# Kernel tuning notes

Measured on AMD Instinct MI355X. Metric: run time of the kernel, lower is better.

The kernel has to match this reference:

```python
import jax, jax.numpy as jnp
import numpy as np

DIM = 128
HEADS = 4
DIM_HEAD = 32
HIDDEN = HEADS * DIM_HEAD  # 128
B, N = 8, 16384


def setup_inputs() -> dict:
    key = jax.random.key(0)
    k1, k2, k3, k4 = jax.random.split(key, 4)
    x = jax.random.normal(k1, (B, DIM, N), dtype=jnp.float32)
    # Conv1d kernels with kernel_size=1 are just [out, in] matrices
    w_qkv = jax.random.normal(k2, (3 * HIDDEN, DIM), dtype=jnp.float32) * (1.0 / np.sqrt(DIM))
    w_out = jax.random.normal(k3, (DIM, HIDDEN), dtype=jnp.float32) * (1.0 / np.sqrt(HIDDEN))
    b_out = jax.random.normal(k4, (DIM,), dtype=jnp.float32) * 0.01
    g = jnp.ones((1, DIM, 1), dtype=jnp.float32)  # RMSNorm gain
    return {"x": x, "w_qkv": w_qkv, "w_out": w_out, "b_out": b_out, "g": g}


def reference(x, w_qkv, w_out, b_out, g):
    b, c, n = x.shape
    scale = DIM_HEAD ** -0.5
    # 1x1 conv projection: [b, 3*hidden, n]
    qkv = jnp.einsum('bcn,oc->bon', x, w_qkv)
    q, k, v = jnp.split(qkv, 3, axis=1)
    # [b, h, d, n]
    q = q.reshape(b, HEADS, DIM_HEAD, n)
    k = k.reshape(b, HEADS, DIM_HEAD, n)
    v = v.reshape(b, HEADS, DIM_HEAD, n)
    q = jax.nn.softmax(q, axis=2) * scale   # softmax over feature dim d
    k = jax.nn.softmax(k, axis=3)            # softmax over sequence dim n
    # linear attention: context [b,h,d,e], then expand back over n
    context = jnp.einsum('bhdn,bhen->bhde', k, v)
    out = jnp.einsum('bhde,bhdn->bhen', context, q)
    out = out.reshape(b, HEADS * DIM_HEAD, n)
    # output 1x1 conv with bias
    out = jnp.einsum('bcn,oc->bon', out, w_out) + b_out[None, :, None]
    # RMSNorm over channel dim (F.normalize dim=1, eps=1e-12)
    nrm = jnp.sqrt(jnp.sum(out * out, axis=1, keepdims=True))
    out = out / jnp.maximum(nrm, 1e-12) * g * jnp.sqrt(jnp.asarray(DIM, out.dtype))
    return out
```

## Files before the change

### kernel.cpp

```cpp
#include <hip/hip_runtime.h>
#include <math.h>

typedef unsigned short ushort_t;
typedef unsigned int uint_t;
typedef __attribute__((ext_vector_type(8))) short short8;
typedef __attribute__((ext_vector_type(4))) float f32x4;
typedef __attribute__((ext_vector_type(4))) uint_t uint4v;
typedef __attribute__((ext_vector_type(2))) uint_t uint2v;

#define NSEQ 16384
#define SCALE_Q 0.17677669529663687f
#define RMS_K 11.313708498984761f

__device__ __forceinline__ ushort_t f2bf(float f) {
  uint_t u = __builtin_bit_cast(uint_t, f);
  u += 0x7FFFu + ((u >> 16) & 1u);
  return (ushort_t)(u >> 16);
}
__device__ __forceinline__ uint_t f2bf2(float lo, float hi) {
  return (uint_t)f2bf(lo) | ((uint_t)f2bf(hi) << 16);
}
__device__ __forceinline__ float bf2f(ushort_t u) {
  return __builtin_bit_cast(float, ((uint_t)u) << 16);
}
__device__ __forceinline__ int swz(int row, int col) {
  int slot = (col >> 3) ^ (row & 7);
  int w2 = ((col >> 1) & 3) ^ (((row >> 4) & 1) << 1);
  return row * 128 + slot * 8 + w2 * 2 + (col & 1);
}
__device__ __forceinline__ short8 ldfrag(const ushort_t* lds, int row, int col8, int pp) {
  int slot = (col8 >> 3) ^ (row & 7);
  const uint4v q = *(const uint4v*)&lds[row * 128 + slot * 8];
  uint4v r;
  if (pp) { r.x = q.z; r.y = q.w; r.z = q.x; r.w = q.y; } else { r = q; }
  return __builtin_bit_cast(short8, r);
}
#define MFMA(a, b, c) __builtin_amdgcn_mfma_f32_16x16x32_bf16((a), (b), (c), 0, 0, 0)

__global__ void kP(const float* __restrict__ w_qkv, const float* __restrict__ w_out,
                   ushort_t* __restrict__ wkv_pk, ushort_t* __restrict__ wq_pk,
                   ushort_t* __restrict__ wout_pk) {
  const int i = blockIdx.x * 256 + threadIdx.x;
  const int j = i & 7, lane = (i >> 3) & 63;
  const int l15 = lane & 15, l4 = lane >> 4;
  if (i < 32768) {
    const int rest = i >> 9, Nt = rest & 15, kk = rest >> 4;
    wkv_pk[i] = f2bf(w_qkv[(128 + Nt * 16 + l15) * 128 + kk * 32 + l4 * 8 + j]);
  } else if (i < 49152) {
    const int i2 = i - 32768, rest = i2 >> 9, Nt = rest & 7, kk = rest >> 3;
    wq_pk[i2] = f2bf(w_qkv[(Nt * 16 + l15) * 128 + kk * 32 + l4 * 8 + j]);
  } else if (i < 65536) {
    const int i2 = i - 49152, rest = i2 >> 9, Nt = rest & 7, kk = rest >> 3;
    wout_pk[i2] = f2bf(w_out[(Nt * 16 + l15) * 128 + kk * 32 + l4 * 8 + j]);
  }
}

__global__ __launch_bounds__(512, 2)
void kA(const float* __restrict__ x, const ushort_t* __restrict__ wkv_pk,
        float* __restrict__ ctx_acc, float* __restrict__ S_glob) {
  __shared__ ushort_t xs[2][16384];
  __shared__ ushort_t eks[16384];
  __shared__ ushort_t vs[16384];
  __shared__ float S_lds[128];
  const int b = blockIdx.y, blk = blockIdx.x;
  const int tid = threadIdx.x, wave = tid >> 6, lane = tid & 63;
  const int mg = wave >> 2, ng = wave & 3;
  const int h = wave >> 1, dt = wave & 1;
  const int l15 = lane & 15, l4 = lane >> 4;
  if (tid < 128) S_lds[tid] = 0.f;

  short8 wf[4][4];
#pragma unroll
  for (int kk = 0; kk < 4; ++kk)
#pragma unroll
    for (int nt = 0; nt < 4; ++nt)
      wf[kk][nt] = *(const short8*)&wkv_pk[((kk * 16 + ng * 4 + nt) * 64 + lane) * 8];

  const f32x4 fzero = {0.f, 0.f, 0.f, 0.f};
  f32x4 cacc[2]; cacc[0] = fzero; cacc[1] = fzero;
  float sacc[4] = {0.f, 0.f, 0.f, 0.f};

  const int sn = tid & 127, cb = (tid >> 7) * 32;
  const float* xb = x + (size_t)b * 128 * NSEQ + blk * 512 + sn;
  float pf[32];
#pragma unroll
  for (int i = 0; i < 32; ++i) pf[i] = xb[(size_t)(cb + i) * NSEQ];

  for (int s = 0; s < 4; ++s) {
    const int p = s & 1;
    __syncthreads();
    {
      uint_t* xw = (uint_t*)xs[p];
#pragma unroll
      for (int i = 0; i < 32; i += 2)
        xw[swz(sn, cb + i) >> 1] = f2bf2(pf[i], pf[i + 1]);
    }
    if (s < 3) {
#pragma unroll
      for (int i = 0; i < 32; ++i) pf[i] = xb[(size_t)(cb + i) * NSEQ + (s + 1) * 128];
    }
    __syncthreads();
    f32x4 pacc[4][4];
#pragma unroll
    for (int mt = 0; mt < 4; ++mt)
#pragma unroll
      for (int nt = 0; nt < 4; ++nt) pacc[mt][nt] = fzero;
#pragma unroll
    for (int kk = 0; kk < 4; ++kk) {
      short8 af[4];
#pragma unroll
      for (int mt = 0; mt < 4; ++mt)
        af[mt] = ldfrag(xs[p], mg * 64 + mt * 16 + l15, kk * 32 + l4 * 8, mt & 1);
#pragma unroll
      for (int mt = 0; mt < 4; ++mt)
#pragma unroll
        for (int nt = 0; nt < 4; ++nt)
          pacc[mt][nt] = MFMA(af[mt], wf[kk][nt], pacc[mt][nt]);
    }
#pragma unroll
    for (int nt = 0; nt < 4; ++nt) {
      const int kvr = ng * 64 + nt * 16 + l15;
#pragma unroll
      for (int mt = 0; mt < 4; ++mt) {
        const int nq = mg * 64 + mt * 16 + l4 * 4;
        f32x4 v = pacc[mt][nt];
        if (ng < 2) {
          float e0 = __expf(v.x), e1 = __expf(v.y), e2 = __expf(v.z), e3 = __expf(v.w);
          sacc[nt] += (e0 + e1) + (e2 + e3);
          uint_t* ew = (uint_t*)eks;
          ew[swz(kvr, nq) >> 1] = f2bf2(e0, e1);
          ew[swz(kvr, nq + 2) >> 1] = f2bf2(e2, e3);
        } else {
          uint_t* vw = (uint_t*)vs;
          vw[swz(kvr - 128, nq) >> 1] = f2bf2(v.x, v.y);
          vw[swz(kvr - 128, nq + 2) >> 1] = f2bf2(v.z, v.w);
        }
      }
    }
    __syncthreads();
    const int drow = h * 32 + dt * 16 + l15;
#pragma unroll
    for (int kk2 = 0; kk2 < 4; ++kk2) {
      short8 ea = ldfrag(eks, drow, kk2 * 32 + l4 * 8, dt);
#pragma unroll
      for (int et = 0; et < 2; ++et) {
        short8 vb = ldfrag(vs, h * 32 + et * 16 + l15, kk2 * 32 + l4 * 8, et);
        cacc[et] = MFMA(ea, vb, cacc[et]);
      }
    }
  }
#pragma unroll
  for (int et = 0; et < 2; ++et) {
    float* dst = &ctx_acc[((((b * 4 + h) * 2 + dt) * 2 + et) * 64 + lane) * 4];
    atomicAdd(dst + 0, cacc[et].x);
    atomicAdd(dst + 1, cacc[et].y);
    atomicAdd(dst + 2, cacc[et].z);
    atomicAdd(dst + 3, cacc[et].w);
  }
  if (ng < 2) {
#pragma unroll
    for (int nt = 0; nt < 4; ++nt)
      atomicAdd(&S_lds[ng * 64 + nt * 16 + l15], sacc[nt]);
  }
  __syncthreads();
  if (tid < 128) atomicAdd(&S_glob[b * 128 + tid], S_lds[tid]);
}

__global__ void kB(const float* __restrict__ ctx_acc, const float* __restrict__ S_glob,
                   ushort_t* __restrict__ ctx_pk) {
  const int bh = blockIdx.x;
  const int b = bh >> 2, hh = bh & 3;
  const int t = threadIdx.x;
  const int lane = t & 63, dtet = t >> 6, dt = dtet >> 1, et = dtet & 1;
  const int l15 = lane & 15, q = lane >> 4;
  const f32x4 c4 = *(const f32x4*)&ctx_acc[(((bh * 2 + dt) * 2 + et) * 64 + lane) * 4];
  const int dbase = dt * 16 + q * 4;
  ushort_t o[4];
#pragma unroll
  for (int r = 0; r < 4; ++r) {
    const float S = S_glob[b * 128 + hh * 32 + dbase + r];
    o[r] = f2bf(c4[r] / S);
  }
  const int lp = l15 + (((dbase >> 3) & 3) << 4);
  uint2v w;
  w.x = (uint_t)o[0] | ((uint_t)o[1] << 16);
  w.y = (uint_t)o[2] | ((uint_t)o[3] << 16);
  *(uint2v*)&ctx_pk[((bh * 2 + et) * 64 + lp) * 8 + (q & 1) * 4] = w;
}

__global__ __launch_bounds__(512, 2)
void kC(const float* __restrict__ x, const ushort_t* __restrict__ wq_pk,
        const ushort_t* __restrict__ wout_pk, const ushort_t* __restrict__ ctx_pk,
        const float* __restrict__ b_out, const float* __restrict__ g,
        float* __restrict__ out) {
  __shared__ ushort_t xs[2][16384];
  __shared__ ushort_t qlog[16384];
  __shared__ ushort_t yT[16384];
  __shared__ float nrm[128];
  __shared__ float bias_l[128], g_l[128];
  const int b = blockIdx.y, blk = blockIdx.x;
  const int tid = threadIdx.x, wave = tid >> 6, lane = tid & 63;
  const int mg = wave >> 1, ng = wave & 1;
  const int l15 = lane & 15, l4 = lane >> 4;
  if (tid < 128) { bias_l[tid] = b_out[tid]; g_l[tid] = g[tid]; }

  short8 cfr[4];
#pragma unroll
  for (int nt = 0; nt < 4; ++nt) {
    const int Nt = ng * 4 + nt, hh = Nt >> 1, et = Nt & 1;
    cfr[nt] = *(const short8*)&ctx_pk[(((b * 4 + hh) * 2 + et) * 64 + lane) * 8];
  }
  const f32x4 fzero = {0.f, 0.f, 0.f, 0.f};
  const int sn = tid & 127, cb = (tid >> 7) * 32;
  const float* xb = x + (size_t)b * 128 * NSEQ + blk * 512 + sn;
  float pf[32];
#pragma unroll
  for (int i = 0; i < 32; ++i) pf[i] = xb[(size_t)(cb + i) * NSEQ];

  for (int s = 0; s < 4; ++s) {
    const int p = s & 1;
    __syncthreads();
    if (tid < 128) nrm[tid] = 0.f;
    {
      uint_t* xw = (uint_t*)xs[p];
#pragma unroll
      for (int i = 0; i < 32; i += 2)
        xw[swz(sn, cb + i) >> 1] = f2bf2(pf[i], pf[i + 1]);
    }
    if (s < 3) {
#pragma unroll
      for (int i = 0; i < 32; ++i) pf[i] = xb[(size_t)(cb + i) * NSEQ + (s + 1) * 128];
    }
    __syncthreads();
    f32x4 pacc[2][4];
#pragma unroll
    for (int mt = 0; mt < 2; ++mt)
#pragma unroll
      for (int nt = 0; nt < 4; ++nt) pacc[mt][nt] = fzero;
#pragma unroll
    for (int kk = 0; kk < 4; ++kk) {
      short8 wqf[4];
#pragma unroll
      for (int nt = 0; nt < 4; ++nt)
        wqf[nt] = *(const short8*)&wq_pk[((kk * 8 + ng * 4 + nt) * 64 + lane) * 8];
      short8 af[2];
#pragma unroll
      for (int mt = 0; mt < 2; ++mt)
        af[mt] = ldfrag(xs[p], mg * 32 + mt * 16 + l15, kk * 32 + l4 * 8, mt & 1);
#pragma unroll
      for (int mt = 0; mt < 2; ++mt)
#pragma unroll
        for (int nt = 0; nt < 4; ++nt)
          pacc[mt][nt] = MFMA(af[mt], wqf[nt], pacc[mt][nt]);
    }
    {
      uint_t* qw = (uint_t*)qlog;
#pragma unroll
      for (int nt = 0; nt < 4; ++nt) {
        const int qrow = ng * 64 + nt * 16 + l15;
#pragma unroll
        for (int mt = 0; mt < 2; ++mt) {
          const int nq = mg * 32 + mt * 16 + l4 * 4;
          qw[swz(qrow, nq) >> 1] = f2bf2(pacc[mt][nt].x, pacc[mt][nt].y);
          qw[swz(qrow, nq + 2) >> 1] = f2bf2(pacc[mt][nt].z, pacc[mt][nt].w);
        }
      }
    }
    __syncthreads();
    {
      const int n2 = tid & 127, hq = tid >> 7;
      float lv[32];
#pragma unroll
      for (int i = 0; i < 32; ++i) lv[i] = bf2f(qlog[swz(hq * 32 + i, n2)]);
      float m = lv[0];
#pragma unroll
      for (int i = 1; i < 32; ++i) m = fmaxf(m, lv[i]);
      float ssum = 0.f;
#pragma unroll
      for (int i = 0; i < 32; ++i) { lv[i] = __expf(lv[i] - m); ssum += lv[i]; }
      const float qs = SCALE_Q / ssum;
      uint_t* hw = (uint_t*)xs[p];
#pragma unroll
      for (int i = 0; i < 32; i += 2)
        hw[swz(n2, hq * 32 + i) >> 1] = f2bf2(lv[i] * qs, lv[i + 1] * qs);
    }
    __syncthreads();
    f32x4 oacc[2][4];
#pragma unroll
    for (int mt = 0; mt < 2; ++mt)
#pragma unroll
      for (int nt = 0; nt < 4; ++nt) oacc[mt][nt] = fzero;
#pragma unroll
    for (int hi = 0; hi < 2; ++hi) {
      const int h2 = ng * 2 + hi;
      short8 af[2];
#pragma unroll
      for (int mt = 0; mt < 2; ++mt)
        af[mt] = ldfrag(xs[p], mg * 32 + mt * 16 + l15, h2 * 32 + l4 * 8, mt & 1);
#pragma unroll
      for (int et = 0; et < 2; ++et) {
        const int nt = hi * 2 + et;
#pragma unroll
        for (int mt = 0; mt < 2; ++mt)
          oacc[mt][nt] = MFMA(af[mt], cfr[nt], oacc[mt][nt]);
      }
    }
    {
      uint_t* yw = (uint_t*)yT;
#pragma unroll
      for (int nt = 0; nt < 4; ++nt) {
        const int hid = ng * 64 + nt * 16 + l15;
        const int hb = hid & ~1;
#pragma unroll
        for (int mt = 0; mt < 2; ++mt) {
          const int nq = mg * 32 + mt * 16 + l4 * 4;
          f32x4 v = oacc[mt][nt];
          float o0 = __shfl_xor(v.x, 1), o1 = __shfl_xor(v.y, 1);
          float o2 = __shfl_xor(v.z, 1), o3 = __shfl_xor(v.w, 1);
          if ((lane & 1) == 0) {
            yw[swz(nq, hb) >> 1] = f2bf2(v.x, o0);
            yw[swz(nq + 1, hb) >> 1] = f2bf2(v.y, o1);
          } else {
            yw[swz(nq + 2, hb) >> 1] = f2bf2(o2, v.z);
            yw[swz(nq + 3, hb) >> 1] = f2bf2(o3, v.w);
          }
        }
      }
    }
    __syncthreads();
    f32x4 facc[2][4];
#pragma unroll
    for (int mt = 0; mt < 2; ++mt)
#pragma unroll
      for (int nt = 0; nt < 4; ++nt) facc[mt][nt] = fzero;
#pragma unroll
    for (int kk = 0; kk < 4; ++kk) {
      short8 wof[4];
#pragma unroll
      for (int nt = 0; nt < 4; ++nt)
        wof[nt] = *(const short8*)&wout_pk[((kk * 8 + ng * 4 + nt) * 64 + lane) * 8];
      short8 af[2];
#pragma unroll
      for (int mt = 0; mt < 2; ++mt)
        af[mt] = ldfrag(yT, mg * 32 + mt * 16 + l15, kk * 32 + l4 * 8, mt & 1);
#pragma unroll
      for (int mt = 0; mt < 2; ++mt)
#pragma unroll
        for (int nt = 0; nt < 4; ++nt)
          facc[mt][nt] = MFMA(af[mt], wof[nt], facc[mt][nt]);
    }
    float sq[2][4] = {{0.f, 0.f, 0.f, 0.f}, {0.f, 0.f, 0.f, 0.f}};
#pragma unroll
    for (int nt = 0; nt < 4; ++nt) {
      const int outc = ng * 64 + nt * 16 + l15;
      const float bb = bias_l[outc];
#pragma unroll
      for (int mt = 0; mt < 2; ++mt) {
        facc[mt][nt].x += bb; facc[mt][nt].y += bb;
        facc[mt][nt].z += bb; facc[mt][nt].w += bb;
        sq[mt][0] += facc[mt][nt].x * facc[mt][nt].x;
        sq[mt][1] += facc[mt][nt].y * facc[mt][nt].y;
        sq[mt][2] += facc[mt][nt].z * facc[mt][nt].z;
        sq[mt][3] += facc[mt][nt].w * facc[mt][nt].w;
      }
    }
#pragma unroll
    for (int mt = 0; mt < 2; ++mt)
#pragma unroll
      for (int r = 0; r < 4; ++r) {
        sq[mt][r] += __shfl_xor(sq[mt][r], 1);
        sq[mt][r] += __shfl_xor(sq[mt][r], 2);
        sq[mt][r] += __shfl_xor(sq[mt][r], 4);
        sq[mt][r] += __shfl_xor(sq[mt][r], 8);
      }
    if (l15 == 0) {
#pragma unroll
      for (int mt = 0; mt < 2; ++mt)
#pragma unroll
        for (int r = 0; r < 4; ++r)
          atomicAdd(&nrm[mg * 32 + mt * 16 + l4 * 4 + r], sq[mt][r]);
    }
    __syncthreads();
#pragma unroll
    for (int mt = 0; mt < 2; ++mt) {
      const int nq = mg * 32 + mt * 16 + l4 * 4;
      const float inv0 = RMS_K / fmaxf(sqrtf(nrm[nq + 0]), 1e-12f);
      const float inv1 = RMS_K / fmaxf(sqrtf(nrm[nq + 1]), 1e-12f);
      const float inv2 = RMS_K / fmaxf(sqrtf(nrm[nq + 2]), 1e-12f);
      const float inv3 = RMS_K / fmaxf(sqrtf(nrm[nq + 3]), 1e-12f);
#pragma unroll
      for (int nt = 0; nt < 4; ++nt) {
        const int outc = ng * 64 + nt * 16 + l15;
        const float gg = g_l[outc];
        f32x4 o;
        o.x = facc[mt][nt].x * inv0 * gg;
        o.y = facc[mt][nt].y * inv1 * gg;
        o.z = facc[mt][nt].z * inv2 * gg;
        o.w = facc[mt][nt].w * inv3 * gg;
        *(f32x4*)&out[(size_t)(b * 128 + outc) * NSEQ + blk * 512 + s * 128 + nq] = o;
      }
    }
  }
}

extern "C" void kernel_launch(void* const* d_in, const int* in_sizes, int n_in,
                              void* d_out, int out_size, void* d_ws, size_t ws_size,
                              hipStream_t stream) {
  const float* x = (const float*)d_in[0];
  const float* w_qkv = (const float*)d_in[1];
  const float* w_out = (const float*)d_in[2];
  const float* b_out = (const float*)d_in[3];
  const float* g = (const float*)d_in[4];
  float* out = (float*)d_out;

  float* ctx_acc = (float*)d_ws;
  float* S_glob = ctx_acc + 32768;
  ushort_t* wkv_pk = (ushort_t*)(S_glob + 1024);
  ushort_t* wq_pk = wkv_pk + 32768;
  ushort_t* wout_pk = wq_pk + 16384;
  ushort_t* ctx_pk = wout_pk + 16384;

  hipMemsetAsync(d_ws, 0, (32768 + 1024) * sizeof(float), stream);
  hipLaunchKernelGGL(kP, dim3(256), dim3(256), 0, stream, w_qkv, w_out, wkv_pk, wq_pk, wout_pk);
  hipLaunchKernelGGL(kA, dim3(32, 8), dim3(512), 0, stream, x, wkv_pk, ctx_acc, S_glob);
  hipLaunchKernelGGL(kB, dim3(32), dim3(256), 0, stream, ctx_acc, S_glob, ctx_pk);
  hipLaunchKernelGGL(kC, dim3(32, 8), dim3(512), 0, stream, x, wq_pk, wout_pk, ctx_pk, b_out, g, out);
}
```

Measured before the change: 288.9 us.

## Halve per-step tile to 64 positions, double grid, raise occupancy to four blocks

The per-block sequence chunk in kA and kC drops from 512 to 256 positions, processed in 64-position steps. The x double buffer becomes a single buffer and new 64-wide swizzle helpers are added, shrinking LDS so four 512-thread blocks can fit per CU. The grid doubles to 64x8, and kC switches x loads and output stores to nontemporal hints. This targets low occupancy and poor latency hiding on the memory-bound streaming passes, at the cost of more context atomics, less work per wave and losing the double-buffered x staging.

```diff
diff --git a/kernel.cpp b/kernel.cpp
--- a/kernel.cpp
+++ b/kernel.cpp
@@ -23,14 +23,26 @@
 __device__ __forceinline__ float bf2f(ushort_t u) {
   return __builtin_bit_cast(float, ((uint_t)u) << 16);
 }
-__device__ __forceinline__ int swz(int row, int col) {
+__device__ __forceinline__ int swzA(int row, int col) {
   int slot = (col >> 3) ^ (row & 7);
   int w2 = ((col >> 1) & 3) ^ (((row >> 4) & 1) << 1);
   return row * 128 + slot * 8 + w2 * 2 + (col & 1);
 }
-__device__ __forceinline__ short8 ldfrag(const ushort_t* lds, int row, int col8, int pp) {
+__device__ __forceinline__ int swzB(int row, int col) {
+  int slot = ((col >> 3) & 7) ^ (row & 7);
+  int w2 = ((col >> 1) & 3) ^ (((row >> 4) & 1) << 1);
+  return row * 64 + slot * 8 + w2 * 2 + (col & 1);
+}
+__device__ __forceinline__ short8 ldfragA(const ushort_t* lds, int row, int col8, int pp) {
   int slot = (col8 >> 3) ^ (row & 7);
   const uint4v q = *(const uint4v*)&lds[row * 128 + slot * 8];
+  uint4v r;
+  if (pp) { r.x = q.z; r.y = q.w; r.z = q.x; r.w = q.y; } else { r = q; }
+  return __builtin_bit_cast(short8, r);
+}
+__device__ __forceinline__ short8 ldfragB(const ushort_t* lds, int row, int col8, int pp) {
+  int slot = ((col8 >> 3) & 7) ^ (row & 7);
+  const uint4v q = *(const uint4v*)&lds[row * 64 + slot * 8];
   uint4v r;
   if (pp) { r.x = q.z; r.y = q.w; r.z = q.x; r.w = q.y; } else { r = q; }
   return __builtin_bit_cast(short8, r);
@@ -55,12 +67,12 @@
   }
 }
 
-__global__ __launch_bounds__(512, 2)
+__global__ __launch_bounds__(512, 4)
 void kA(const float* __restrict__ x, const ushort_t* __restrict__ wkv_pk,
         float* __restrict__ ctx_acc, float* __restrict__ S_glob) {
-  __shared__ ushort_t xs[2][16384];
-  __shared__ ushort_t eks[16384];
-  __shared__ ushort_t vs[16384];
+  __shared__ ushort_t xs[64 * 128];
+  __shared__ ushort_t eks[128 * 64];
+  __shared__ ushort_t vs[128 * 64];
   __shared__ float S_lds[128];
   const int b = blockIdx.y, blk = blockIdx.x;
   const int tid = threadIdx.x, wave = tid >> 6, lane = tid & 63;
@@ -80,39 +92,38 @@
   f32x4 cacc[2]; cacc[0] = fzero; cacc[1] = fzero;
   float sacc[4] = {0.f, 0.f, 0.f, 0.f};
 
-  const int sn = tid & 127, cb = (tid >> 7) * 32;
-  const float* xb = x + (size_t)b * 128 * NSEQ + blk * 512 + sn;
-  float pf[32];
-#pragma unroll
-  for (int i = 0; i < 32; ++i) pf[i] = xb[(size_t)(cb + i) * NSEQ];
+  const int sn = tid & 63, cb = (tid >> 6) * 16;
+  const float* xb = x + (size_t)b * 128 * NSEQ + blk * 256 + sn;
+  float pf[16];
+#pragma unroll
+  for (int i = 0; i < 16; ++i) pf[i] = xb[(size_t)(cb + i) * NSEQ];
 
   for (int s = 0; s < 4; ++s) {
-    const int p = s & 1;
     __syncthreads();
     {
-      uint_t* xw = (uint_t*)xs[p];
-#pragma unroll
-      for (int i = 0; i < 32; i += 2)
-        xw[swz(sn, cb + i) >> 1] = f2bf2(pf[i], pf[i + 1]);
+      uint_t* xw = (uint_t*)xs;
+#pragma unroll
+      for (int i = 0; i < 16; i += 2)
+        xw[swzA(sn, cb + i) >> 1] = f2bf2(pf[i], pf[i + 1]);
     }
     if (s < 3) {
 #pragma unroll
-      for (int i = 0; i < 32; ++i) pf[i] = xb[(size_t)(cb + i) * NSEQ + (s + 1) * 128];
-    }
-    __syncthreads();
-    f32x4 pacc[4][4];
-#pragma unroll
-    for (int mt = 0; mt < 4; ++mt)
+      for (int i = 0; i < 16; ++i) pf[i] = xb[(size_t)(cb + i) * NSEQ + (s + 1) * 64];
+    }
+    __syncthreads();
+    f32x4 pacc[2][4];
+#pragma unroll
+    for (int mt = 0; mt < 2; ++mt)
 #pragma unroll
       for (int nt = 0; nt < 4; ++nt) pacc[mt][nt] = fzero;
 #pragma unroll
     for (int kk = 0; kk < 4; ++kk) {
-      short8 af[4];
-#pragma unroll
-      for (int mt = 0; mt < 4; ++mt)
-        af[mt] = ldfrag(xs[p], mg * 64 + mt * 16 + l15, kk * 32 + l4 * 8, mt & 1);
-#pragma unroll
-      for (int mt = 0; mt < 4; ++mt)
+      short8 af[2];
+#pragma unroll
+      for (int mt = 0; mt < 2; ++mt)
+        af[mt] = ldfragA(xs, mg * 32 + mt * 16 + l15, kk * 32 + l4 * 8, mt & 1);
+#pragma unroll
+      for (int mt = 0; mt < 2; ++mt)
 #pragma unroll
         for (int nt = 0; nt < 4; ++nt)
           pacc[mt][nt] = MFMA(af[mt], wf[kk][nt], pacc[mt][nt]);
@@ -121,30 +132,30 @@
     for (int nt = 0; nt < 4; ++nt) {
       const int kvr = ng * 64 + nt * 16 + l15;
 #pragma unroll
-      for (int mt = 0; mt < 4; ++mt) {
-        const int nq = mg * 64 + mt * 16 + l4 * 4;
+      for (int mt = 0; mt < 2; ++mt) {
+        const int nq = mg * 32 + mt * 16 + l4 * 4;
         f32x4 v = pacc[mt][nt];
         if (ng < 2) {
           float e0 = __expf(v.x), e1 = __expf(v.y), e2 = __expf(v.z), e3 = __expf(v.w);
           sacc[nt] += (e0 + e1) + (e2 + e3);
           uint_t* ew = (uint_t*)eks;
-          ew[swz(kvr, nq) >> 1] = f2bf2(e0, e1);
-          ew[swz(kvr, nq + 2) >> 1] = f2bf2(e2, e3);
+          ew[swzB(kvr, nq) >> 1] = f2bf2(e0, e1);
+          ew[swzB(kvr, nq + 2) >> 1] = f2bf2(e2, e3);
         } else {
           uint_t* vw = (uint_t*)vs;
-          vw[swz(kvr - 128, nq) >> 1] = f2bf2(v.x, v.y);
-          vw[swz(kvr - 128, nq + 2) >> 1] = f2bf2(v.z, v.w);
+          vw[swzB(kvr - 128, nq) >> 1] = f2bf2(v.x, v.y);
+          vw[swzB(kvr - 128, nq + 2) >> 1] = f2bf2(v.z, v.w);
         }
       }
     }
     __syncthreads();
     const int drow = h * 32 + dt * 16 + l15;
 #pragma unroll
-    for (int kk2 = 0; kk2 < 4; ++kk2) {
-      short8 ea = ldfrag(eks, drow, kk2 * 32 + l4 * 8, dt);
+    for (int kk2 = 0; kk2 < 2; ++kk2) {
+      short8 ea = ldfragB(eks, drow, kk2 * 32 + l4 * 8, dt);
 #pragma unroll
       for (int et = 0; et < 2; ++et) {
-        short8 vb = ldfrag(vs, h * 32 + et * 16 + l15, kk2 * 32 + l4 * 8, et);
+        short8 vb = ldfragB(vs, h * 32 + et * 16 + l15, kk2 * 32 + l4 * 8, et);
         cacc[et] = MFMA(ea, vb, cacc[et]);
       }
     }
@@ -188,15 +199,15 @@
   *(uint2v*)&ctx_pk[((bh * 2 + et) * 64 + lp) * 8 + (q & 1) * 4] = w;
 }
 
-__global__ __launch_bounds__(512, 2)
+__global__ __launch_bounds__(512, 4)
 void kC(const float* __restrict__ x, const ushort_t* __restrict__ wq_pk,
         const ushort_t* __restrict__ wout_pk, const ushort_t* __restrict__ ctx_pk,
         const float* __restrict__ b_out, const float* __restrict__ g,
         float* __restrict__ out) {
-  __shared__ ushort_t xs[2][16384];
-  __shared__ ushort_t qlog[16384];
-  __shared__ ushort_t yT[16384];
-  __shared__ float nrm[128];
+  __shared__ ushort_t xs[64 * 128];
+  __shared__ ushort_t qlog[128 * 64];
+  __shared__ ushort_t yT[64 * 128];
+  __shared__ float nrm[64];
   __shared__ float bias_l[128], g_l[128];
   const int b = blockIdx.y, blk = blockIdx.x;
   const int tid = threadIdx.x, wave = tid >> 6, lane = tid & 63;
@@ -211,67 +222,57 @@
     cfr[nt] = *(const short8*)&ctx_pk[(((b * 4 + hh) * 2 + et) * 64 + lane) * 8];
   }
   const f32x4 fzero = {0.f, 0.f, 0.f, 0.f};
-  const int sn = tid & 127, cb = (tid >> 7) * 32;
-  const float* xb = x + (size_t)b * 128 * NSEQ + blk * 512 + sn;
-  float pf[32];
-#pragma unroll
-  for (int i = 0; i < 32; ++i) pf[i] = xb[(size_t)(cb + i) * NSEQ];
+  const int sn = tid & 63, cb = (tid >> 6) * 16;
+  const float* xb = x + (size_t)b * 128 * NSEQ + blk * 256 + sn;
+  float pf[16];
+#pragma unroll
+  for (int i = 0; i < 16; ++i) pf[i] = __builtin_nontemporal_load(&xb[(size_t)(cb + i) * NSEQ]);
 
   for (int s = 0; s < 4; ++s) {
-    const int p = s & 1;
-    __syncthreads();
-    if (tid < 128) nrm[tid] = 0.f;
+    __syncthreads();
+    if (tid < 64) nrm[tid] = 0.f;
     {
-      uint_t* xw = (uint_t*)xs[p];
-#pragma unroll
-      for (int i = 0; i < 32; i += 2)
-        xw[swz(sn, cb + i) >> 1] = f2bf2(pf[i], pf[i + 1]);
+      uint_t* xw = (uint_t*)xs;
+#pragma unroll
+      for (int i = 0; i < 16; i += 2)
+        xw[swzA(sn, cb + i) >> 1] = f2bf2(pf[i], pf[i + 1]);
     }
     if (s < 3) {
 #pragma unroll
-      for (int i = 0; i < 32; ++i) pf[i] = xb[(size_t)(cb + i) * NSEQ + (s + 1) * 128];
-    }
-    __syncthreads();
-    f32x4 pacc[2][4];
-#pragma unroll
-    for (int mt = 0; mt < 2; ++mt)
-#pragma unroll
-      for (int nt = 0; nt < 4; ++nt) pacc[mt][nt] = fzero;
+      for (int i = 0; i < 16; ++i)
+        pf[i] = __builtin_nontemporal_load(&xb[(size_t)(cb + i) * NSEQ + (s + 1) * 64]);
+    }
+    __syncthreads();
+    f32x4 pacc[4];
+#pragma unroll
+    for (int nt = 0; nt < 4; ++nt) pacc[nt] = fzero;
 #pragma unroll
     for (int kk = 0; kk < 4; ++kk) {
       short8 wqf[4];
 #pragma unroll
       for (int nt = 0; nt < 4; ++nt)
         wqf[nt] = *(const short8*)&wq_pk[((kk * 8 + ng * 4 + nt) * 64 + lane) * 8];
-      short8 af[2];
-#pragma unroll
-      for (int mt = 0; mt < 2; ++mt)
-        af[mt] = ldfrag(xs[p], mg * 32 + mt * 16 + l15, kk * 32 + l4 * 8, mt & 1);
-#pragma unroll
-      for (int mt = 0; mt < 2; ++mt)
-#pragma unroll
-        for (int nt = 0; nt < 4; ++nt)
-          pacc[mt][nt] = MFMA(af[mt], wqf[nt], pacc[mt][nt]);
+      short8 af = ldfragA(xs, mg * 16 + l15, kk * 32 + l4 * 8, mg & 1);
+#pragma unroll
+      for (int nt = 0; nt < 4; ++nt)
+        pacc[nt] = MFMA(af, wqf[nt], pacc[nt]);
     }
     {
       uint_t* qw = (uint_t*)qlog;
 #pragma unroll
       for (int nt = 0; nt < 4; ++nt) {
         const int qrow = ng * 64 + nt * 16 + l15;
-#pragma unroll
-        for (int mt = 0; mt < 2; ++mt) {
-          const int nq = mg * 32 + mt * 16 + l4 * 4;
-          qw[swz(qrow, nq) >> 1] = f2bf2(pacc[mt][nt].x, pacc[mt][nt].y);
-          qw[swz(qrow, nq + 2) >> 1] = f2bf2(pacc[mt][nt].z, pacc[mt][nt].w);
-        }
-      }
-    }
-    __syncthreads();
-    {
-      const int n2 = tid & 127, hq = tid >> 7;
+        const int nq = mg * 16 + l4 * 4;
+        qw[swzB(qrow, nq) >> 1] = f2bf2(pacc[nt].x, pacc[nt].y);
+        qw[swzB(qrow, nq + 2) >> 1] = f2bf2(pacc[nt].z, pacc[nt].w);
+      }
+    }
+    __syncthreads();
+    if (tid < 256) {
+      const int n2 = tid & 63, hq = tid >> 6;
       float lv[32];
 #pragma unroll
-      for (int i = 0; i < 32; ++i) lv[i] = bf2f(qlog[swz(hq * 32 + i, n2)]);
+      for (int i = 0; i < 32; ++i) lv[i] = bf2f(qlog[swzB(hq * 32 + i, n2)]);
       float m = lv[0];
 #pragma unroll
       for (int i = 1; i < 32; ++i) m = fmaxf(m, lv[i]);
@@ -279,30 +280,23 @@
 #pragma unroll
       for (int i = 0; i < 32; ++i) { lv[i] = __expf(lv[i] - m); ssum += lv[i]; }
       const float qs = SCALE_Q / ssum;
-      uint_t* hw = (uint_t*)xs[p];
+      uint_t* hw = (uint_t*)xs;
 #pragma unroll
       for (int i = 0; i < 32; i += 2)
-        hw[swz(n2, hq * 32 + i) >> 1] = f2bf2(lv[i] * qs, lv[i + 1] * qs);
-    }
-    __syncthreads();
-    f32x4 oacc[2][4];
-#pragma unroll
-    for (int mt = 0; mt < 2; ++mt)
-#pragma unroll
-      for (int nt = 0; nt < 4; ++nt) oacc[mt][nt] = fzero;
+        hw[swzA(n2, hq * 32 + i) >> 1] = f2bf2(lv[i] * qs, lv[i + 1] * qs);
+    }
+    __syncthreads();
+    f32x4 oacc[4];
+#pragma unroll
+    for (int nt = 0; nt < 4; ++nt) oacc[nt] = fzero;
 #pragma unroll
     for (int hi = 0; hi < 2; ++hi) {
       const int h2 = ng * 2 + hi;
-      short8 af[2];
-#pragma unroll
-      for (int mt = 0; mt < 2; ++mt)
-        af[mt] = ldfrag(xs[p], mg * 32 + mt * 16 + l15, h2 * 32 + l4 * 8, mt & 1);
+      short8 af = ldfragA(xs, mg * 16 + l15, h2 * 32 + l4 * 8, mg & 1);
 #pragma unroll
       for (int et = 0; et < 2; ++et) {
         const int nt = hi * 2 + et;
-#pragma unroll
-        for (int mt = 0; mt < 2; ++mt)
-          oacc[mt][nt] = MFMA(af[mt], cfr[nt], oacc[mt][nt]);
+        oacc[nt] = MFMA(af, cfr[nt], oacc[nt]);
       }
     }
     {
@@ -311,79 +305,61 @@
       for (int nt = 0; nt < 4; ++nt) {
         const int hid = ng * 64 + nt * 16 + l15;
         const int hb = hid & ~1;
-#pragma unroll
-        for (int mt = 0; mt < 2; ++mt) {
-          const int nq = mg * 32 + mt * 16 + l4 * 4;
-          f32x4 v = oacc[mt][nt];
-          float o0 = __shfl_xor(v.x, 1), o1 = __shfl_xor(v.y, 1);
-          float o2 = __shfl_xor(v.z, 1), o3 = __shfl_xor(v.w, 1);
-          if ((lane & 1) == 0) {
-            yw[swz(nq, hb) >> 1] = f2bf2(v.x, o0);
-            yw[swz(nq + 1, hb) >> 1] = f2bf2(v.y, o1);
-          } else {
-            yw[swz(nq + 2, hb) >> 1] = f2bf2(o2, v.z);
-            yw[swz(nq + 3, hb) >> 1] = f2bf2(o3, v.w);
-          }
+        const int nq = mg * 16 + l4 * 4;
+        f32x4 v = oacc[nt];
+        float o0 = __shfl_xor(v.x, 1), o1 = __shfl_xor(v.y, 1);
+        float o2 = __shfl_xor(v.z, 1), o3 = __shfl_xor(v.w, 1);
+        if ((lane & 1) == 0) {
+          yw[swzA(nq, hb) >> 1] = f2bf2(v.x, o0);
+          yw[swzA(nq + 1, hb) >> 1] = f2bf2(v.y, o1);
+        } else {
+          yw[swzA(nq + 2, hb) >> 1] = f2bf2(o2, v.z);
+          yw[swzA(nq + 3, hb) >> 1] = f2bf2(o3, v.w);
         }
       }
     }
     __syncthreads();
-    f32x4 facc[2][4];
-#pragma unroll
-    for (int mt = 0; mt < 2; ++mt)
-#pragma unroll
-      for (int nt = 0; nt < 4; ++nt) facc[mt][nt] = fzero;
+    f32x4 facc[4];
+#pragma unroll
+    for (int nt = 0; nt < 4; ++nt) facc[nt] = fzero;
 #pragma unroll
     for (int kk = 0; kk < 4; ++kk) {
       short8 wof[4];
 #pragma unroll
       for (int nt = 0; nt < 4; ++nt)
         wof[nt] = *(const short8*)&wout_pk[((kk * 8 + ng * 4 + nt) * 64 + lane) * 8];
-      short8 af[2];
-#pragma unroll
-      for (int mt = 0; mt < 2; ++mt)
-        af[mt] = ldfrag(yT, mg * 32 + mt * 16 + l15, kk * 32 + l4 * 8, mt & 1);
-#pragma unroll
-      for (int mt = 0; mt < 2; ++mt)
-#pragma unroll
-        for (int nt = 0; nt < 4; ++nt)
-          facc[mt][nt] = MFMA(af[mt], wof[nt], facc[mt][nt]);
-    }
-    float sq[2][4] = {{0.f, 0.f, 0.f, 0.f}, {0.f, 0.f, 0.f, 0.f}};
+      short8 af = ldfragA(yT, mg * 16 + l15, kk * 32 + l4 * 8, mg & 1);
+#pragma unroll
+      for (int nt = 0; nt < 4; ++nt)
+        facc[nt] = MFMA(af, wof[nt], facc[nt]);
+    }
+    float sq[4] = {0.f, 0.f, 0.f, 0.f};
 #pragma unroll
     for (int nt = 0; nt < 4; ++nt) {
       const int outc = ng * 64 + nt * 16 + l15;
       const float bb = bias_l[outc];
-#pragma unroll
-      for (int mt = 0; mt < 2; ++mt) {
-        facc[mt][nt].x += bb; facc[mt][nt].y += bb;
-        facc[mt][nt].z += bb; facc[mt][nt].w += bb;
-        sq[mt][0] += facc[mt][nt].x * facc[mt][nt].x;
-        sq[mt][1] += facc[mt][nt].y * facc[mt][nt].y;
-        sq[mt][2] += facc[mt][nt].z * facc[mt][nt].z;
-        sq[mt][3] += facc[mt][nt].w * facc[mt][nt].w;
-      }
-    }
-#pragma unroll
-    for (int mt = 0; mt < 2; ++mt)
-#pragma unroll
-      for (int r = 0; r < 4; ++r) {
-        sq[mt][r] += __shfl_xor(sq[mt][r], 1);
-        sq[mt][r] += __shfl_xor(sq[mt][r], 2);
-        sq[mt][r] += __shfl_xor(sq[mt][r], 4);
-        sq[mt][r] += __shfl_xor(sq[mt][r], 8);
-      }
+      facc[nt].x += bb; facc[nt].y += bb;
+      facc[nt].z += bb; facc[nt].w += bb;
+      sq[0] += facc[nt].x * facc[nt].x;
+      sq[1] += facc[nt].y * facc[nt].y;
+      sq[2] += facc[nt].z * facc[nt].z;
+      sq[3] += facc[nt].w * facc[nt].w;
+    }
+#pragma unroll
+    for (int r = 0; r < 4; ++r) {
+      sq[r] += __shfl_xor(sq[r], 1);
+      sq[r] += __shfl_xor(sq[r], 2);
+      sq[r] += __shfl_xor(sq[r], 4);
+      sq[r] += __shfl_xor(sq[r], 8);
+    }
     if (l15 == 0) {
 #pragma unroll
-      for (int mt = 0; mt < 2; ++mt)
-#pragma unroll
-        for (int r = 0; r < 4; ++r)
-          atomicAdd(&nrm[mg * 32 + mt * 16 + l4 * 4 + r], sq[mt][r]);
-    }
-    __syncthreads();
-#pragma unroll
-    for (int mt = 0; mt < 2; ++mt) {
-      const int nq = mg * 32 + mt * 16 + l4 * 4;
+      for (int r = 0; r < 4; ++r)
+        atomicAdd(&nrm[mg * 16 + l4 * 4 + r], sq[r]);
+    }
+    __syncthreads();
+    {
+      const int nq = mg * 16 + l4 * 4;
       const float inv0 = RMS_K / fmaxf(sqrtf(nrm[nq + 0]), 1e-12f);
       const float inv1 = RMS_K / fmaxf(sqrtf(nrm[nq + 1]), 1e-12f);
       const float inv2 = RMS_K / fmaxf(sqrtf(nrm[nq + 2]), 1e-12f);
@@ -393,11 +369,12 @@
         const int outc = ng * 64 + nt * 16 + l15;
         const float gg = g_l[outc];
         f32x4 o;
-        o.x = facc[mt][nt].x * inv0 * gg;
-        o.y = facc[mt][nt].y * inv1 * gg;
-        o.z = facc[mt][nt].z * inv2 * gg;
-        o.w = facc[mt][nt].w * inv3 * gg;
-        *(f32x4*)&out[(size_t)(b * 128 + outc) * NSEQ + blk * 512 + s * 128 + nq] = o;
+        o.x = facc[nt].x * inv0 * gg;
+        o.y = facc[nt].y * inv1 * gg;
+        o.z = facc[nt].z * inv2 * gg;
+        o.w = facc[nt].w * inv3 * gg;
+        __builtin_nontemporal_store(o,
+            (f32x4*)&out[(size_t)(b * 128 + outc) * NSEQ + blk * 256 + s * 64 + nq]);
       }
     }
   }
@@ -422,7 +399,7 @@
 
   hipMemsetAsync(d_ws, 0, (32768 + 1024) * sizeof(float), stream);
   hipLaunchKernelGGL(kP, dim3(256), dim3(256), 0, stream, w_qkv, w_out, wkv_pk, wq_pk, wout_pk);
-  hipLaunchKernelGGL(kA, dim3(32, 8), dim3(512), 0, stream, x, wkv_pk, ctx_acc, S_glob);
+  hipLaunchKernelGGL(kA, dim3(64, 8), dim3(512), 0, stream, x, wkv_pk, ctx_acc, S_glob);
   hipLaunchKernelGGL(kB, dim3(32), dim3(256), 0, stream, ctx_acc, S_glob, ctx_pk);
-  hipLaunchKernelGGL(kC, dim3(32, 8), dim3(512), 0, stream, x, wq_pk, wout_pk, ctx_pk, b_out, g, out);
-}
+  hipLaunchKernelGGL(kC, dim3(64, 8), dim3(512), 0, stream, x, wq_pk, wout_pk, ctx_pk, b_out, g, out);
+}
```

After: 362.6 us. 25.5% more time.
